# Performance work log

Measured on AMD Instinct MI355X. Metric: run time of the kernel, lower is better.

Reference implementation:

```python
import jax, jax.numpy as jnp
import numpy as np

N_OBJ, N_SR, N_V, N_F = 8192, 4096, 4100, 4096
EPS = 1e-8


def setup_inputs() -> dict:
    key = jax.random.key(0)
    k1, k2, k3, k4, k5 = jax.random.split(key, 5)
    obj_points = jax.random.normal(k1, (N_OBJ, 3), jnp.float32)
    sr_points = 0.5 * jax.random.normal(k2, (N_SR, 3), jnp.float32)
    hand_verts = 0.5 * jax.random.normal(k3, (N_V, 3), jnp.float32)
    face_normals = jax.random.normal(k4, (N_F, 3), jnp.float32)
    hand_faces = jax.random.randint(k5, (N_F, 3), 0, N_V)
    return dict(obj_points=obj_points, sr_points=sr_points,
                hand_verts=hand_verts, face_normals=face_normals,
                hand_faces=hand_faces)


def reference(obj_points, sr_points, hand_verts, face_normals, hand_faces):
    # --- get_NN: brute-force nearest hand point for every object point ---
    d2 = (jnp.sum(obj_points**2, -1)[:, None]
          + jnp.sum(sr_points**2, -1)[None, :]
          - 2.0 * obj_points @ sr_points.T)          # [N, M] squared dists
    nn_idx = jnp.argmin(d2, axis=1)                   # [N]
    trg_pts = sr_points[nn_idx]                       # batched_index_select -> [N,3]
    D = trg_pts - obj_points                          # ray directions [N,3]

    # --- ray-triangle intersection (plane test + 3 edge half-plane tests) ---
    # All [F,N,3] intermediates are avoided via triple-product expansion:
    # every quantity reduces to einsums of per-face [F,3] with per-ray [N,3].
    tri = hand_verts[hand_faces]                      # [F,3,3]
    v0, v1, v2 = tri[:, 0], tri[:, 1], tri[:, 2]
    n = face_normals                                  # [F,3]

    denom = jnp.einsum('fk,nk->fn', n, D)             # D . n   [F,N]
    num = jnp.sum(v0 * n, -1)[:, None] - jnp.einsum('fk,nk->fn', n, obj_points)
    dmask = jnp.abs(denom) > EPS
    t = num / jnp.where(dmask, denom, 1.0)            # plane hit parameter [F,N]

    def edge_sign(va, vb):
        # ((vb-va) x (P-va)) . n  with  P = O + t*D, expanded bilinearly
        c = jnp.cross(n, vb - va)                     # [F,3]
        base = (jnp.einsum('fk,nk->fn', c, obj_points)
                - jnp.sum(va * c, -1)[:, None])
        return base + t * jnp.einsum('fk,nk->fn', c, D)

    inside = ((edge_sign(v0, v1) >= 0)
              & (edge_sign(v1, v2) >= 0)
              & (edge_sign(v2, v0) >= 0))
    hit = inside & dmask & (t > EPS)                  # [F,N]

    hit_number = jnp.sum(hit.astype(jnp.int32), axis=0)   # per ray [N]
    interior = (hit_number % 2) != 0                        # odd parity -> inside

    diff = trg_pts - obj_points
    pen_dist = jnp.sqrt(jnp.sum(diff**2 * interior[:, None].astype(diff.dtype)) + 1e-12)

    # --- contact_map_of_m_to_n(obj_points, sr_points) ---
    nn_dist = jnp.sqrt(jnp.maximum(jnp.min(d2, axis=1), 0.0))
    cmap = 1.0 - 2.0 * (jax.nn.sigmoid(100.0 * nn_dist) - 0.5)

    return pen_dist, cmap
```

## Files before the change

kernel.cpp:

```cpp
#include <hip/hip_runtime.h>
#include <math.h>

#define N_OBJ 8192
#define N_SR  4096
#define N_F   4096
#define EPSF  1e-8f

typedef float v2f __attribute__((ext_vector_type(2)));
static __device__ __forceinline__ v2f sp(float x) { v2f r; r.x = x; r.y = x; return r; }
static __device__ __forceinline__ v2f vfma(v2f a, v2f b, v2f c) { return __builtin_elementwise_fma(a, b, c); }
static __device__ __forceinline__ v2f vmin2(v2f a, v2f b) { return __builtin_elementwise_min(a, b); }

__global__ void __launch_bounds__(256) nn_all(const float* __restrict__ obj,
                                              const float* __restrict__ sr,
                                              const float* __restrict__ hv,
                                              const float* __restrict__ fn,
                                              const int* __restrict__ hf,
                                              float* __restrict__ out,
                                              float4* __restrict__ Dws,
                                              int* __restrict__ hits,
                                              float4* __restrict__ F,
                                              int* __restrict__ done) {
    __shared__ float4 pXY[N_SR / 2];
    __shared__ float4 pZS[N_SR / 2];
    const int tid = threadIdx.x, b = blockIdx.x;

    const float2* sr2 = (const float2*)sr;
#pragma unroll
    for (int i = 0; i < 8; ++i) {
        int e = i * 256 + tid;
        float2 A = sr2[3 * e], B = sr2[3 * e + 1], C = sr2[3 * e + 2];
        float x0 = A.x, y0 = A.y, z0 = B.x, x1 = B.y, y1 = C.x, z1 = C.y;
        float s0 = fmaf(x0, x0, fmaf(y0, y0, z0 * z0));
        float s1 = fmaf(x1, x1, fmaf(y1, y1, z1 * z1));
        pXY[e] = make_float4(x0, x1, y0, y1);
        pZS[e] = make_float4(z0, z1, s0, s1);
    }
    if (tid < 16) hits[b * 16 + tid] = 0;
    if (b == 0 && tid == 0) done[0] = 0;
    if (tid < 8) {
        const int f = b * 8 + tid;
        const int i0 = hf[3*f], i1 = hf[3*f+1], i2 = hf[3*f+2];
        const float v0x = hv[3*i0], v0y = hv[3*i0+1], v0z = hv[3*i0+2];
        const float v1x = hv[3*i1], v1y = hv[3*i1+1], v1z = hv[3*i1+2];
        const float v2x = hv[3*i2], v2y = hv[3*i2+1], v2z = hv[3*i2+2];
        const float nx = fn[3*f], ny = fn[3*f+1], nz = fn[3*f+2];
        F[4*f+0] = make_float4(nx, ny, nz, v0x*nx + v0y*ny + v0z*nz);
        {
            float ex = v1x-v0x, ey = v1y-v0y, ez = v1z-v0z;
            float cx = ny*ez-nz*ey, cy = nz*ex-nx*ez, cz = nx*ey-ny*ex;
            F[4*f+1] = make_float4(cx, cy, cz, v0x*cx + v0y*cy + v0z*cz);
        }
        {
            float ex = v2x-v1x, ey = v2y-v1y, ez = v2z-v1z;
            float cx = ny*ez-nz*ey, cy = nz*ex-nx*ez, cz = nx*ey-ny*ex;
            F[4*f+2] = make_float4(cx, cy, cz, v1x*cx + v1y*cy + v1z*cz);
        }
        {
            float ex = v0x-v2x, ey = v0y-v2y, ez = v0z-v2z;
            float cx = ny*ez-nz*ey, cy = nz*ex-nx*ez, cz = nx*ey-ny*ex;
            F[4*f+3] = make_float4(cx, cy, cz, v2x*cx + v2y*cy + v2z*cz);
        }
    }
    __syncthreads();

    const int w = tid >> 6, lane = tid & 63;
    const int pbase = b * 16 + w * 4;

    float ox[4], oy[4], oz[4], aa[4];
#pragma unroll
    for (int k = 0; k < 4; ++k) {
        int p = pbase + k;
        ox[k] = obj[3*p]; oy[k] = obj[3*p+1]; oz[k] = obj[3*p+2];
        aa[k] = fmaf(ox[k], ox[k], fmaf(oy[k], oy[k], oz[k] * oz[k]));
    }
    float b0[4], b1[4]; int i0[4], i1[4];
#pragma unroll
    for (int k = 0; k < 4; ++k) { b0[k] = b1[k] = INFINITY; i0[k] = 0; i1[k] = 1; }

    int e2 = lane * 2;
#pragma unroll 4
    for (int step = 0; step < 32; ++step) {
        int e = step * 64 + lane;
        float4 A = pXY[e];
        float4 B = pZS[e];
        v2f X; X.x = A.x; X.y = A.y;
        v2f Y; Y.x = A.z; Y.y = A.w;
        v2f Z; Z.x = B.x; Z.y = B.y;
        v2f SS; SS.x = B.z; SS.y = B.w;
#pragma unroll
        for (int k = 0; k < 4; ++k) {
            v2f d  = vfma(Z, sp(oz[k]), vfma(Y, sp(oy[k]), X * sp(ox[k])));
            v2f d2 = vfma(d, sp(-2.f), SS);
            bool c0 = d2.x < b0[k];
            bool c1 = d2.y < b1[k];
            b0[k] = c0 ? d2.x : b0[k];  i0[k] = c0 ? e2     : i0[k];
            b1[k] = c1 ? d2.y : b1[k];  i1[k] = c1 ? e2 + 1 : i1[k];
        }
        e2 += 128;
    }
#pragma unroll
    for (int k = 0; k < 4; ++k) {
        float bd = b0[k]; int bi = i0[k];
        if (b1[k] < bd || (b1[k] == bd && i1[k] < bi)) { bd = b1[k]; bi = i1[k]; }
#pragma unroll
        for (int off = 32; off > 0; off >>= 1) {
            float d = __shfl_down(bd, off);
            int   i = __shfl_down(bi, off);
            if (d < bd || (d == bd && i < bi)) { bd = d; bi = i; }
        }
        if (lane == 0) {
            int p = pbase + k;
            float4 A = pXY[bi >> 1];
            float4 B = pZS[bi >> 1];
            int h = bi & 1;
            float sx = h ? A.y : A.x;
            float sy = h ? A.w : A.z;
            float sz = h ? B.y : B.x;
            float dx = sx - ox[k], dy = sy - oy[k], dz = sz - oz[k];
            Dws[p] = make_float4(dx, dy, dz, fmaf(dx, dx, fmaf(dy, dy, dz * dz)));
            float nn  = sqrtf(fmaxf(bd + aa[k], 0.f));
            float sig = 1.f / (1.f + expf(-100.f * nn));
            out[1 + p] = 1.f - 2.f * (sig - 0.5f);
        }
    }
}

#define RFC 32
#define RAY_NB 512
__global__ void __launch_bounds__(256) ray_count(const float* __restrict__ obj,
                                                 const float4* __restrict__ Dws,
                                                 const float4* __restrict__ F,
                                                 int* __restrict__ hits,
                                                 int* __restrict__ done,
                                                 float* __restrict__ out) {
    __shared__ float4 sF[RFC * 4];
    __shared__ float wsum[4];
    __shared__ int lastf;
    const int tid = threadIdx.x;
    const int pg = blockIdx.x & 3, fc = blockIdx.x >> 2;

    v2f px[4], py[4], pz[4], qx[4], qy[4], qz[4];
    int cnt[8];
#pragma unroll
    for (int g = 0; g < 4; ++g) {
#pragma unroll
        for (int h = 0; h < 2; ++h) {
            int p = pg * 2048 + (g * 2 + h) * 256 + tid;
            px[g][h] = obj[3*p]; py[g][h] = obj[3*p+1]; pz[g][h] = obj[3*p+2];
            float4 D = Dws[p];
            qx[g][h] = D.x; qy[g][h] = D.y; qz[g][h] = D.z;
            cnt[g * 2 + h] = 0;
        }
    }
    {
        const float* Ff = (const float*)(F + (size_t)fc * RFC * 4);
        float* sf = (float*)sF;
#pragma unroll
        for (int i = 0; i < RFC * 16 / 256; ++i)
            sf[i * 256 + tid] = Ff[i * 256 + tid];
    }
    __syncthreads();

#pragma unroll 2
    for (int f = 0; f < RFC; ++f) {
        const float4 Fn = sF[4*f+0];
        const float4 C1 = sF[4*f+1];
        const float4 C2 = sF[4*f+2];
        const float4 C3 = sF[4*f+3];
#pragma unroll
        for (int g = 0; g < 4; ++g) {
            v2f denom = vfma(sp(Fn.z), qz[g], vfma(sp(Fn.y), qy[g], sp(Fn.x) * qx[g]));
            v2f num   = sp(Fn.w) - vfma(sp(Fn.z), pz[g], vfma(sp(Fn.y), py[g], sp(Fn.x) * px[g]));
            v2f dn = __builtin_elementwise_abs(denom);
            v2f nm = __builtin_elementwise_copysign(num, num * denom);
            v2f wx = vfma(px[g], dn, nm * qx[g]);
            v2f wy = vfma(py[g], dn, nm * qy[g]);
            v2f wz = vfma(pz[g], dn, nm * qz[g]);
            v2f q1 = vfma(sp(-C1.w), dn, vfma(sp(C1.z), wz, vfma(sp(C1.y), wy, sp(C1.x) * wx)));
            v2f q2 = vfma(sp(-C2.w), dn, vfma(sp(C2.z), wz, vfma(sp(C2.y), wy, sp(C2.x) * wx)));
            v2f q3 = vfma(sp(-C3.w), dn, vfma(sp(C3.z), wz, vfma(sp(C3.y), wy, sp(C3.x) * wx)));
            v2f mm = vmin2(q1, vmin2(q2, q3));
            mm = vmin2(mm, vfma(sp(-EPSF), dn, nm));
            mm = vmin2(mm, dn - sp(EPSF));
            cnt[g * 2 + 0] += (mm[0] >= 0.f) ? 1 : 0;
            cnt[g * 2 + 1] += (mm[1] >= 0.f) ? 1 : 0;
        }
    }
#pragma unroll
    for (int g = 0; g < 8; ++g)
        atomicAdd(&hits[pg * 2048 + g * 256 + tid], cnt[g]);

    __syncthreads();
    if (tid == 0) {
        __threadfence();
        lastf = (atomicAdd(done, 1) == RAY_NB - 1) ? 1 : 0;
    }
    __syncthreads();
    if (lastf) {
        float s = 0.f;
#pragma unroll 8
        for (int k = tid; k < N_OBJ; k += 256) {
            int h = atomicAdd(&hits[k], 0);
            if (h & 1) s += Dws[k].w;
        }
#pragma unroll
        for (int off = 32; off > 0; off >>= 1) s += __shfl_down(s, off);
        if ((tid & 63) == 0) wsum[tid >> 6] = s;
        __syncthreads();
        if (tid == 0)
            out[0] = sqrtf(wsum[0] + wsum[1] + wsum[2] + wsum[3] + 1e-12f);
    }
}

extern "C" void kernel_launch(void* const* d_in, const int* in_sizes, int n_in,
                              void* d_out, int out_size, void* d_ws, size_t ws_size,
                              hipStream_t stream) {
    const float* obj = (const float*)d_in[0];
    const float* sr  = (const float*)d_in[1];
    const float* hv  = (const float*)d_in[2];
    const float* fn  = (const float*)d_in[3];
    const int*   hf  = (const int*)d_in[4];
    float* out = (float*)d_out;

    char* ws = (char*)d_ws;
    float4* Dws  = (float4*)(ws + 0);
    int*    hits = (int*)  (ws + 131072);
    float4* F    = (float4*)(ws + 163840);
    int*    done = (int*)  (ws + 425984);

    nn_all<<<512, 256, 0, stream>>>(obj, sr, hv, fn, hf, out, Dws, hits, F, done);
    ray_count<<<RAY_NB, 256, 0, stream>>>(obj, Dws, F, hits, done, out);
}
```

Baseline: 115.4 us.

## Replace atomic hit accumulation with per-chunk byte counts and separate finalize kernel

The ray-count kernel now handles 64 faces per block over 1024 rays, down from 32 faces over 2048. It prefetches the next face's coefficients from shared memory into registers. Instead of doing atomicAdd into a global hits array and running a last-block reduction, each block writes per-ray counts as bytes into a partial-count buffer. A new 32-block finalize kernel sums the 64 chunk counts per ray, reduces the masked squared distances, and combines the block partials through a done counter. This removes global atomics and the serial last-block tail, at the cost of an extra kernel launch and a 512KB intermediate buffer.

```diff
diff --git a/kernel.cpp b/kernel.cpp
--- a/kernel.cpp
+++ b/kernel.cpp
@@ -18,7 +18,6 @@
                                               const int* __restrict__ hf,
                                               float* __restrict__ out,
                                               float4* __restrict__ Dws,
-                                              int* __restrict__ hits,
                                               float4* __restrict__ F,
                                               int* __restrict__ done) {
     __shared__ float4 pXY[N_SR / 2];
@@ -36,7 +35,6 @@
         pXY[e] = make_float4(x0, x1, y0, y1);
         pZS[e] = make_float4(z0, z1, s0, s1);
     }
-    if (tid < 16) hits[b * 16 + tid] = 0;
     if (b == 0 && tid == 0) done[0] = 0;
     if (tid < 8) {
         const int f = b * 8 + tid;
@@ -126,27 +124,22 @@
     }
 }
 
-#define RFC 32
-#define RAY_NB 512
+#define RFC 64
 __global__ void __launch_bounds__(256) ray_count(const float* __restrict__ obj,
                                                  const float4* __restrict__ Dws,
                                                  const float4* __restrict__ F,
-                                                 int* __restrict__ hits,
-                                                 int* __restrict__ done,
-                                                 float* __restrict__ out) {
+                                                 unsigned char* __restrict__ pcount) {
     __shared__ float4 sF[RFC * 4];
-    __shared__ float wsum[4];
-    __shared__ int lastf;
     const int tid = threadIdx.x;
-    const int pg = blockIdx.x & 3, fc = blockIdx.x >> 2;
-
-    v2f px[4], py[4], pz[4], qx[4], qy[4], qz[4];
-    int cnt[8];
-#pragma unroll
-    for (int g = 0; g < 4; ++g) {
+    const int pg = blockIdx.x & 7, fc = blockIdx.x >> 3;
+
+    v2f px[2], py[2], pz[2], qx[2], qy[2], qz[2];
+    int cnt[4];
+#pragma unroll
+    for (int g = 0; g < 2; ++g) {
 #pragma unroll
         for (int h = 0; h < 2; ++h) {
-            int p = pg * 2048 + (g * 2 + h) * 256 + tid;
+            int p = pg * 1024 + (g * 2 + h) * 256 + tid;
             px[g][h] = obj[3*p]; py[g][h] = obj[3*p+1]; pz[g][h] = obj[3*p+2];
             float4 D = Dws[p];
             qx[g][h] = D.x; qy[g][h] = D.y; qz[g][h] = D.z;
@@ -162,14 +155,15 @@
     }
     __syncthreads();
 
-#pragma unroll 2
+    float4 nF0 = sF[0], nF1 = sF[1], nF2 = sF[2], nF3 = sF[3];
+#pragma unroll 4
     for (int f = 0; f < RFC; ++f) {
-        const float4 Fn = sF[4*f+0];
-        const float4 C1 = sF[4*f+1];
-        const float4 C2 = sF[4*f+2];
-        const float4 C3 = sF[4*f+3];
-#pragma unroll
-        for (int g = 0; g < 4; ++g) {
+        const float4 Fn = nF0, C1 = nF1, C2 = nF2, C3 = nF3;
+        if (f + 1 < RFC) {
+            nF0 = sF[4*f+4]; nF1 = sF[4*f+5]; nF2 = sF[4*f+6]; nF3 = sF[4*f+7];
+        }
+#pragma unroll
+        for (int g = 0; g < 2; ++g) {
             v2f denom = vfma(sp(Fn.z), qz[g], vfma(sp(Fn.y), qy[g], sp(Fn.x) * qx[g]));
             v2f num   = sp(Fn.w) - vfma(sp(Fn.z), pz[g], vfma(sp(Fn.y), py[g], sp(Fn.x) * px[g]));
             v2f dn = __builtin_elementwise_abs(denom);
@@ -188,28 +182,39 @@
         }
     }
 #pragma unroll
-    for (int g = 0; g < 8; ++g)
-        atomicAdd(&hits[pg * 2048 + g * 256 + tid], cnt[g]);
-
+    for (int g = 0; g < 4; ++g)
+        pcount[(size_t)fc * N_OBJ + pg * 1024 + g * 256 + tid] = (unsigned char)cnt[g];
+}
+
+__global__ void __launch_bounds__(256) finalize(const float4* __restrict__ Dws,
+                                                const unsigned char* __restrict__ pcount,
+                                                float* __restrict__ fpart,
+                                                int* __restrict__ done,
+                                                float* __restrict__ out) {
+    __shared__ float wsum[4];
+    __shared__ int lastf;
+    const int tid = threadIdx.x;
+    const int pt = blockIdx.x * 256 + tid;
+
+    int c = 0;
+#pragma unroll 8
+    for (int fc = 0; fc < 64; ++fc)
+        c += pcount[(size_t)fc * N_OBJ + pt];
+    float s = (c & 1) ? Dws[pt].w : 0.f;
+#pragma unroll
+    for (int off = 32; off > 0; off >>= 1) s += __shfl_down(s, off);
+    if ((tid & 63) == 0) wsum[tid >> 6] = s;
     __syncthreads();
     if (tid == 0) {
+        fpart[blockIdx.x] = wsum[0] + wsum[1] + wsum[2] + wsum[3];
         __threadfence();
-        lastf = (atomicAdd(done, 1) == RAY_NB - 1) ? 1 : 0;
-    }
-    __syncthreads();
-    if (lastf) {
-        float s = 0.f;
-#pragma unroll 8
-        for (int k = tid; k < N_OBJ; k += 256) {
-            int h = atomicAdd(&hits[k], 0);
-            if (h & 1) s += Dws[k].w;
-        }
-#pragma unroll
-        for (int off = 32; off > 0; off >>= 1) s += __shfl_down(s, off);
-        if ((tid & 63) == 0) wsum[tid >> 6] = s;
-        __syncthreads();
-        if (tid == 0)
-            out[0] = sqrtf(wsum[0] + wsum[1] + wsum[2] + wsum[3] + 1e-12f);
+        lastf = (atomicAdd(done, 1) == 31) ? 1 : 0;
+        if (lastf) {
+            float tot = 0.f;
+            for (int i = 0; i < 32; ++i)
+                tot += atomicAdd(&fpart[i], 0.f);
+            out[0] = sqrtf(tot + 1e-12f);
+        }
     }
 }
 
@@ -224,11 +229,13 @@
     float* out = (float*)d_out;
 
     char* ws = (char*)d_ws;
-    float4* Dws  = (float4*)(ws + 0);
-    int*    hits = (int*)  (ws + 131072);
-    float4* F    = (float4*)(ws + 163840);
-    int*    done = (int*)  (ws + 425984);
-
-    nn_all<<<512, 256, 0, stream>>>(obj, sr, hv, fn, hf, out, Dws, hits, F, done);
-    ray_count<<<RAY_NB, 256, 0, stream>>>(obj, Dws, F, hits, done, out);
-}
+    float4*        Dws    = (float4*)(ws + 0);
+    float4*        F      = (float4*)(ws + 131072);
+    unsigned char* pcount = (unsigned char*)(ws + 393216);
+    float*         fpart  = (float*)(ws + 917504);
+    int*           done   = (int*)  (ws + 917632);
+
+    nn_all<<<512, 256, 0, stream>>>(obj, sr, hv, fn, hf, out, Dws, F, done);
+    ray_count<<<512, 256, 0, stream>>>(obj, Dws, F, pcount);
+    finalize<<<32, 256, 0, stream>>>(Dws, pcount, fpart, done, out);
+}
```

Measured after the change: 114.7 us. No clear change (-0.7%).
